# Kernel tuning notes

Measured on AMD Instinct MI355X. Metric: run time of the kernel, lower is better.

## Reference

```python
import jax, jax.numpy as jnp
import numpy as np
from jax import lax

F_DIM = 128
H_DIM = 128
K_NN = 16
S_PTS = 512
EPS = 1e-5


def _layernorm(x, g, b):
    m = jnp.mean(x, -1, keepdims=True)
    v = jnp.mean((x - m) ** 2, -1, keepdims=True)
    return (x - m) * lax.rsqrt(v + EPS) * g + b


def _batchnorm(x, g, b):
    # training-mode BN over (batch, points, neighbors) per channel; x: [B,S,K,C]
    m = jnp.mean(x, (0, 1, 2))
    v = jnp.mean((x - m) ** 2, (0, 1, 2))
    return (x - m) * lax.rsqrt(v + EPS) * g + b


def _gather(x, idx):
    # x: [B,R,C], idx: [B,...] int -> [B,...,C]
    return jax.vmap(lambda a, i: a[i])(x, idx)


def _fps(xyz, S):
    # farthest point sampling, deterministic start at index 0 (pytorch3d default)
    B, N, _ = xyz.shape
    idx0 = jnp.zeros((B,), jnp.int32)

    def step(carry, _):
        mind, last = carry
        p = jax.vmap(lambda a, i: a[i])(xyz, last)  # [B,3]
        d = jnp.sum((xyz - p[:, None]) ** 2, -1)  # [B,N]
        mind = jnp.minimum(mind, d)
        nxt = jnp.argmax(mind, -1).astype(jnp.int32)
        return (mind, nxt), nxt

    init = (jnp.full((B, N), 1e10, xyz.dtype), idx0)
    _, rest = lax.scan(step, init, None, length=S - 1)
    return jnp.concatenate([idx0[None], rest], 0).T  # [B,S]


def _knn_idx(q, ref, K):
    # squared dists [B,Q,R]; top-K nearest, sorted ascending by distance
    d2 = (jnp.sum(q * q, -1)[:, :, None] + jnp.sum(ref * ref, -1)[:, None, :]
          - 2.0 * jnp.einsum('bqd,brd->bqr', q, ref))
    _, idx = lax.top_k(-d2, K)
    return idx


def setup_inputs() -> dict:
    key = jax.random.key(0)
    ks = jax.random.split(key, 32)
    B, N, F, H = 4, 8192, F_DIM, H_DIM
    w = lambda k, shp: (jax.random.normal(k, shp, jnp.float32) * 0.02)
    return {
        'xyzp': jax.random.uniform(ks[0], (B, N, 4), jnp.float32),
        'features': jax.random.normal(ks[1], (B, N, F), jnp.float32),
        'ln_g': jnp.ones((F,), jnp.float32), 'ln_b': jnp.zeros((F,), jnp.float32),
        'td_w0': w(ks[2], (F + 3, F)), 'td_b0': jnp.zeros((F,), jnp.float32),
        'td_bn0_g': jnp.ones((F,), jnp.float32), 'td_bn0_b': jnp.zeros((F,), jnp.float32),
        'td_w1': w(ks[3], (F, F)), 'td_b1': jnp.zeros((F,), jnp.float32),
        'td_bn1_g': jnp.ones((F,), jnp.float32), 'td_bn1_b': jnp.zeros((F,), jnp.float32),
        'w_kern': w(ks[4], (F, H)), 'b_kern': jnp.zeros((H,), jnp.float32),
        'w_gkern': w(ks[5], (F, H)), 'b_gkern': jnp.zeros((H,), jnp.float32),
        'w_agg': w(ks[6], (H, F)), 'b_agg': jnp.zeros((F,), jnp.float32),
        'w_q': w(ks[7], (H, H)), 'w_k': w(ks[8], (H, H)), 'w_v': w(ks[9], (H, H)),
        'pe_w1': w(ks[10], (4, H)), 'pe_b1': jnp.zeros((H,), jnp.float32),
        'pe_w2': w(ks[11], (H, H)), 'pe_b2': jnp.zeros((H,), jnp.float32),
        'at_w1': w(ks[12], (H, H)), 'at_b1': jnp.zeros((H,), jnp.float32),
        'at_w2': w(ks[13], (H, H)), 'at_b2': jnp.zeros((H,), jnp.float32),
    }


def reference(xyzp, features, ln_g, ln_b, td_w0, td_b0, td_bn0_g, td_bn0_b,
              td_w1, td_b1, td_bn1_g, td_bn1_b, w_kern, b_kern, w_gkern, b_gkern,
              w_agg, b_agg, w_q, w_k, w_v, pe_w1, pe_b1, pe_w2, pe_b2,
              at_w1, at_b1, at_w2, at_b2):
    feats = _layernorm(features, ln_g, ln_b)
    xyz = xyzp[:, :, :3]
    # ---- TransitionDown ----
    fps_idx = _fps(xyz, S_PTS)                       # [B,S]
    new_xyz = _gather(xyz, fps_idx)                  # [B,S,3]
    idx_dn = _knn_idx(new_xyz, xyz, K_NN)            # [B,S,K]
    new_xyzp = _gather(xyzp, idx_dn)[:, :, 0]        # [B,S,4] nearest = self
    grouped_xyz = _gather(xyz, idx_dn) - new_xyz[:, :, None]   # [B,S,K,3]
    grouped_feat = _gather(feats, idx_dn)            # [B,S,K,F]
    h = jnp.concatenate([grouped_xyz, grouped_feat], -1)
    h = jax.nn.relu(_batchnorm(h @ td_w0 + td_b0, td_bn0_g, td_bn0_b))
    h = jax.nn.relu(_batchnorm(h @ td_w1 + td_b1, td_bn1_g, td_bn1_b))
    new_feats = jnp.max(h, axis=2)                   # [B,S,F]
    # ---- vector attention over K global neighbors ----
    idx_up = _knn_idx(xyz, new_xyz, K_NN)            # [B,N,K]
    pdiff = xyzp[:, :, None] - _gather(new_xyzp, idx_up)  # [B,N,K,4]
    pos_enc = jax.nn.relu(pdiff @ pe_w1 + pe_b1) @ pe_w2 + pe_b2
    x = feats @ w_kern + b_kern                      # [B,N,H]
    new_x = new_feats @ w_gkern + b_gkern            # [B,S,H]
    q = x @ w_q
    k = _gather(new_x @ w_k, idx_up)                 # [B,N,K,H]
    v = _gather(new_x @ w_v, idx_up)
    a = q[:, :, None] - k + pos_enc
    a = jax.nn.relu(a @ at_w1 + at_b1) @ at_w2 + at_b2
    a = jax.nn.softmax(a / np.float32(np.sqrt(H_DIM)), axis=2)  # softmax over neighbors
    res = jnp.sum(a * (v + pos_enc), axis=2)         # einsum bmnf,bmnf->bmf
    return res @ w_agg + b_agg + feats
```

## Files before the change

kernel.cpp:

```cpp
#include <hip/hip_runtime.h>

constexpr int B = 4, N = 8192, S = 512, K = 16, F = 128, H = 128;
constexpr float EPS = 1e-5f;

typedef short v8s __attribute__((ext_vector_type(8)));
typedef float v4f __attribute__((ext_vector_type(4)));

__device__ __forceinline__ short f2bf(float x) {
  union { float f; unsigned u; } v; v.f = x;
  unsigned r = v.u + 0x7fffu + ((v.u >> 16) & 1u);
  return (short)(r >> 16);
}
__device__ __forceinline__ float bf2f(short s) {
  union { unsigned u; float f; } v; v.u = ((unsigned)(unsigned short)s) << 16;
  return v.f;
}

template <int CTRL>
__device__ __forceinline__ float dpp_mov_f(float v) {
  return __int_as_float(__builtin_amdgcn_update_dpp(
      __float_as_int(v), __float_as_int(v), CTRL, 0xF, 0xF, false));
}
template <int CTRL>
__device__ __forceinline__ int dpp_mov_i(int v) {
  return __builtin_amdgcn_update_dpp(v, v, CTRL, 0xF, 0xF, false);
}

__global__ __launch_bounds__(256) void wconv_kernel(
    const float* __restrict__ pe_w2, const float* __restrict__ at_w1,
    const float* __restrict__ at_w2, const float* __restrict__ w_kern,
    const float* __restrict__ w_q, const float* __restrict__ td_w1,
    const float* __restrict__ td_w0, short* __restrict__ wbf) {
  int i = blockIdx.x * 256 + threadIdx.x;
  if (i < 6 * 16384) {
    int m = i >> 14, e = i & 16383;
    const float* src = m == 0 ? pe_w2 : m == 1 ? at_w1 : m == 2 ? at_w2
                     : m == 3 ? w_kern : m == 4 ? w_q : td_w1;
    int kx = e >> 7, n = e & 127;
    wbf[m * 16384 + n * 128 + kx] = f2bf(src[e]);
  } else {
    int e = i - 6 * 16384;
    int n = e / 160, kz = e % 160;
    short v = (kz < 131) ? f2bf(td_w0[kz * 128 + n]) : (short)0;
    wbf[6 * 16384 + n * 160 + kz] = v;
  }
}

__global__ __launch_bounds__(256) void ln_kernel(const float* __restrict__ features,
    const float* __restrict__ g, const float* __restrict__ bta, float* __restrict__ feats) {
  int r = blockIdx.x * 4 + (threadIdx.x >> 6);
  int lane = threadIdx.x & 63;
  const float2* fp = (const float2*)(features + (size_t)r * F);
  float2 v = fp[lane];
  float s = v.x + v.y;
  #pragma unroll
  for (int off = 32; off > 0; off >>= 1) s += __shfl_xor(s, off);
  float m = s * (1.f / F);
  float dx = v.x - m, dy = v.y - m;
  float s2 = dx * dx + dy * dy;
  #pragma unroll
  for (int off = 32; off > 0; off >>= 1) s2 += __shfl_xor(s2, off);
  float rstd = rsqrtf(s2 * (1.f / F) + EPS);
  float2 gg = ((const float2*)g)[lane];
  float2 bb = ((const float2*)bta)[lane];
  float2* op = (float2*)(feats + (size_t)r * F);
  op[lane] = make_float2(dx * rstd * gg.x + bb.x, dy * rstd * gg.y + bb.y);
}

__global__ __launch_bounds__(256, 1) void fps_kernel(const float* __restrict__ xyzp,
    float* __restrict__ new_xyz) {
  __shared__ float4 xl4[N];
  __shared__ float nx[S * 3];
  __shared__ float2 slot[2][4];
  int b = blockIdx.x, t = threadIdx.x;
  int lane = t & 63, wid = t >> 6;
  const float4* xp = (const float4*)(xyzp + (size_t)b * N * 4);
  float px[32], py[32], pz[32], mind[32];
  #pragma unroll
  for (int j = 0; j < 32; j++) {
    int idx = t + 256 * j;
    float4 p = xp[idx];
    px[j] = p.x; py[j] = p.y; pz[j] = p.z; mind[j] = 1e10f;
    xl4[idx] = p;
  }
  __syncthreads();
  float4 p0 = xl4[0];
  float cx = p0.x, cy = p0.y, cz = p0.z;
  if (t == 0) { nx[0] = cx; nx[1] = cy; nx[2] = cz; }
  for (int s = 1; s < S; ++s) {
    #pragma unroll
    for (int j = 0; j < 32; j++) {
      float dx = __fsub_rn(px[j], cx), dy = __fsub_rn(py[j], cy), dz = __fsub_rn(pz[j], cz);
      float d = __fadd_rn(__fadd_rn(__fmul_rn(dx, dx), __fmul_rn(dy, dy)), __fmul_rn(dz, dz));
      mind[j] = fminf(mind[j], d);
    }
    float a0 = fmaxf(mind[0], mind[1]),   a1 = fmaxf(mind[2], mind[3]);
    float a2 = fmaxf(mind[4], mind[5]),   a3 = fmaxf(mind[6], mind[7]);
    float a4 = fmaxf(mind[8], mind[9]),   a5 = fmaxf(mind[10], mind[11]);
    float a6 = fmaxf(mind[12], mind[13]), a7 = fmaxf(mind[14], mind[15]);
    float a8 = fmaxf(mind[16], mind[17]), a9 = fmaxf(mind[18], mind[19]);
    float aa = fmaxf(mind[20], mind[21]), ab = fmaxf(mind[22], mind[23]);
    float ac = fmaxf(mind[24], mind[25]), ad = fmaxf(mind[26], mind[27]);
    float ae = fmaxf(mind[28], mind[29]), af = fmaxf(mind[30], mind[31]);
    float b0 = fmaxf(a0, a1), b1 = fmaxf(a2, a3), b2 = fmaxf(a4, a5), b3 = fmaxf(a6, a7);
    float b4 = fmaxf(a8, a9), b5 = fmaxf(aa, ab), b6 = fmaxf(ac, ad), b7 = fmaxf(ae, af);
    float c0 = fmaxf(b0, b1), c1 = fmaxf(b2, b3), c2 = fmaxf(b4, b5), c3 = fmaxf(b6, b7);
    float e0 = fmaxf(c0, c1), e1 = fmaxf(c2, c3);
    float bv = fmaxf(e0, e1);
    unsigned msk = 0;
    #pragma unroll
    for (int j = 0; j < 32; j++) msk |= (mind[j] == bv) ? (1u << j) : 0u;
    int bj = __builtin_ctz(msk);
    int bi = t + (bj << 8);
    #define FPS_STEP(CTRL) { \
      float ov = dpp_mov_f<CTRL>(bv); int oi = dpp_mov_i<CTRL>(bi); \
      if (ov > bv || (ov == bv && oi < bi)) { bv = ov; bi = oi; } }
    FPS_STEP(0x111) FPS_STEP(0x112) FPS_STEP(0x114) FPS_STEP(0x118)
    FPS_STEP(0x142) FPS_STEP(0x143)
    #undef FPS_STEP
    int par = s & 1;
    if (lane == 63) slot[par][wid] = make_float2(bv, __int_as_float(bi));
    __syncthreads();
    float2 s0 = slot[par][0], s1 = slot[par][1], s2 = slot[par][2], s3 = slot[par][3];
    int i0 = __float_as_int(s0.y), i1 = __float_as_int(s1.y);
    int i2 = __float_as_int(s2.y), i3 = __float_as_int(s3.y);
    float4 c0v = xl4[i0], c1v = xl4[i1], c2v = xl4[i2], c3v = xl4[i3];
    float v0 = s0.x, v1 = s1.x, v2 = s2.x, v3 = s3.x;
    bool m01 = (v1 > v0) || (v1 == v0 && i1 < i0);
    float va = m01 ? v1 : v0; int ia = m01 ? i1 : i0;
    bool m23 = (v3 > v2) || (v3 == v2 && i3 < i2);
    float vb = m23 ? v3 : v2; int ib = m23 ? i3 : i2;
    bool mf = (vb > va) || (vb == va && ib < ia);
    float cax = m01 ? c1v.x : c0v.x, cay = m01 ? c1v.y : c0v.y, caz = m01 ? c1v.z : c0v.z;
    float cbx = m23 ? c3v.x : c2v.x, cby = m23 ? c3v.y : c2v.y, cbz = m23 ? c3v.z : c2v.z;
    cx = mf ? cbx : cax; cy = mf ? cby : cay; cz = mf ? cbz : caz;
    if (t == 0) { nx[s * 3 + 0] = cx; nx[s * 3 + 1] = cy; nx[s * 3 + 2] = cz; }
  }
  __syncthreads();
  for (int i = t; i < S * 3; i += 256)
    new_xyz[(size_t)b * S * 3 + i] = nx[i];
}

__global__ __launch_bounds__(256) void knn_dn_kernel(const float* __restrict__ xyzp,
    const float* __restrict__ new_xyz, int* __restrict__ idx_dn, float* __restrict__ new_xyzp) {
  int wave = threadIdx.x >> 6, lane = threadIdx.x & 63;
  int qid = blockIdx.x * 4 + wave;
  int b = qid >> 9, s = qid & (S - 1);
  const float4* xp = (const float4*)(xyzp + (size_t)b * N * 4);
  float qx = new_xyz[((size_t)b * S + s) * 3 + 0];
  float qy = new_xyz[((size_t)b * S + s) * 3 + 1];
  float qz = new_xyz[((size_t)b * S + s) * 3 + 2];
  float qq = __fadd_rn(__fadd_rn(__fmul_rn(qx, qx), __fmul_rn(qy, qy)), __fmul_rn(qz, qz));

  float lastD = -1.f; int lastI = -1;
  float curD; int curI;
  auto scan = [&]() {
    curD = 3e38f; curI = 0x7fffffff;
    for (int j = 0; j < 128; j++) {
      int i = lane + 64 * j;
      float4 p = xp[i];
      float rr  = __fadd_rn(__fadd_rn(__fmul_rn(p.x, p.x), __fmul_rn(p.y, p.y)), __fmul_rn(p.z, p.z));
      float dot = __fadd_rn(__fadd_rn(__fmul_rn(qx, p.x), __fmul_rn(qy, p.y)), __fmul_rn(qz, p.z));
      float d2 = __fsub_rn(__fadd_rn(qq, rr), __fmul_rn(2.0f, dot));
      bool gate   = (d2 > lastD) || (d2 == lastD && i > lastI);
      bool better = (d2 < curD) || (d2 == curD && i < curI);
      if (gate && better) { curD = d2; curI = i; }
    }
  };
  scan();
  int outI = 0;
  float4 nn0;
  #pragma unroll 1
  for (int r = 0; r < K; r++) {
    float mD = curD; int mI = curI; int mL = lane;
    #pragma unroll
    for (int off = 32; off > 0; off >>= 1) {
      float od = __shfl_xor(mD, off); int oi = __shfl_xor(mI, off); int ol = __shfl_xor(mL, off);
      if (od < mD || (od == mD && oi < mI)) { mD = od; mI = oi; mL = ol; }
    }
    if (lane == r) outI = mI;
    if (r == 0 && lane == 0) nn0 = xp[mI];
    if (lane == mL) { lastD = mD; lastI = mI; scan(); }
  }
  size_t base = ((size_t)b * S + s) * K;
  if (lane < K) idx_dn[base + lane] = outI;
  if (lane == 0) *(float4*)&new_xyzp[((size_t)b * S + s) * 4] = nn0;
}

__global__ __launch_bounds__(256) void knn_up_kernel(const float* __restrict__ xyzp,
    const float* __restrict__ new_xyz, int* __restrict__ idx_up) {
  int wave = threadIdx.x >> 6, lane = threadIdx.x & 63;
  int qid = blockIdx.x * 4 + wave;
  int b = qid >> 13, n = qid & (N - 1);
  const float4* xp = (const float4*)(xyzp + (size_t)b * N * 4);
  float4 qp = xp[n];
  float qx = qp.x, qy = qp.y, qz = qp.z;
  float qq = __fadd_rn(__fadd_rn(__fmul_rn(qx, qx), __fmul_rn(qy, qy)), __fmul_rn(qz, qz));
  float rx[8], ry[8], rz[8];
  #pragma unroll
  for (int j = 0; j < 8; j++) {
    int i = lane + 64 * j;
    rx[j] = new_xyz[((size_t)b * S + i) * 3 + 0];
    ry[j] = new_xyz[((size_t)b * S + i) * 3 + 1];
    rz[j] = new_xyz[((size_t)b * S + i) * 3 + 2];
  }
  float lastD = -1.f; int lastI = -1;
  float curD; int curI;
  auto scan = [&]() {
    curD = 3e38f; curI = 0x7fffffff;
    #pragma unroll
    for (int j = 0; j < 8; j++) {
      int i = lane + 64 * j;
      float rr  = __fadd_rn(__fadd_rn(__fmul_rn(rx[j], rx[j]), __fmul_rn(ry[j], ry[j])), __fmul_rn(rz[j], rz[j]));
      float dot = __fadd_rn(__fadd_rn(__fmul_rn(qx, rx[j]), __fmul_rn(qy, ry[j])), __fmul_rn(qz, rz[j]));
      float d2 = __fsub_rn(__fadd_rn(qq, rr), __fmul_rn(2.0f, dot));
      bool gate   = (d2 > lastD) || (d2 == lastD && i > lastI);
      bool better = (d2 < curD) || (d2 == curD && i < curI);
      if (gate && better) { curD = d2; curI = i; }
    }
  };
  scan();
  int outI = 0;
  #pragma unroll 1
  for (int r = 0; r < K; r++) {
    float mD = curD; int mI = curI; int mL = lane;
    #pragma unroll
    for (int off = 32; off > 0; off >>= 1) {
      float od = __shfl_xor(mD, off); int oi = __shfl_xor(mI, off); int ol = __shfl_xor(mL, off);
      if (od < mD || (od == mD && oi < mI)) { mD = od; mI = oi; mL = ol; }
    }
    if (lane == r) outI = mI;
    if (lane == mL) { lastD = mD; lastI = mI; scan(); }
  }
  size_t base = ((size_t)b * N + n) * K;
  if (lane < K) idx_up[base + lane] = outI;
}

constexpr int KS0 = 168;
__global__ __launch_bounds__(256) void td0_mfma(const float* __restrict__ xyzp,
    const float* __restrict__ new_xyz, const float* __restrict__ feats,
    const int* __restrict__ idx_dn, const short* __restrict__ w0bf, const float* __restrict__ b0,
    float* __restrict__ act0) {
  __shared__ short WT[128 * KS0];
  __shared__ short Abuf[4][16 * KS0];
  __shared__ int nbs[4][16];
  const int t = threadIdx.x, w = t >> 6, lane = t & 63;
  const int c0 = lane & 15, quad = lane >> 4;
  const int row0 = blockIdx.x * 64 + w * 16;
  const int bI = row0 >> 13;
  if (lane < 16) {
    int nb = idx_dn[row0 + lane];
    nbs[w][lane] = nb;
    int s = ((row0 + lane) >> 4) & (S - 1);
    #pragma unroll
    for (int d = 0; d < 3; d++)
      Abuf[w][lane * KS0 + d] =
          f2bf(xyzp[((size_t)bI * N + nb) * 4 + d] - new_xyz[((size_t)bI * S + s) * 3 + d]);
    for (int k2 = 131; k2 < 160; k2++) Abuf[w][lane * KS0 + k2] = 0;
  }
  #pragma unroll 4
  for (int i = 0; i < 32; i++) {
    int idx = lane + 64 * i;
    int r = idx >> 7, c = idx & 127;
    int nb = nbs[w][r];
    Abuf[w][r * KS0 + 3 + c] = f2bf(feats[((size_t)bI * N + nb) * F + c]);
  }
  #pragma unroll
  for (int i = 0; i < 10; i++) {
    int u = t + 256 * i;
    int n = u / 20, k8 = u % 20;
    *(v8s*)&WT[n * KS0 + k8 * 8] = *(const v8s*)&w0bf[n * 160 + k8 * 8];
  }
  __syncthreads();
  v4f acc[8];
  #pragma unroll
  for (int nt = 0; nt < 8; nt++) { float bvv = b0[nt * 16 + c0]; acc[nt] = (v4f){bvv, bvv, bvv, bvv}; }
  #pragma unroll
  for (int ks = 0; ks < 5; ks++) {
    v8s a = *(const v8s*)&Abuf[w][c0 * KS0 + ks * 32 + quad * 8];
    #pragma unroll
    for (int nt = 0; nt < 8; nt++) {
      v8s bf = *(const v8s*)&WT[(nt * 16 + c0) * KS0 + ks * 32 + quad * 8];
      acc[nt] = __builtin_amdgcn_mfma_f32_16x16x32_bf16(a, bf, acc[nt], 0, 0, 0);
    }
  }
  #pragma unroll
  for (int nt = 0; nt < 8; nt++)
    #pragma unroll
    for (int r = 0; r < 4; r++)
      act0[(size_t)(row0 + quad * 4 + r) * F + nt * 16 + c0] = acc[nt][r];
}

__global__ __launch_bounds__(256) void bn_reduce_kernel(const float* __restrict__ x,
                                                        float* __restrict__ sums) {
  __shared__ float ls[256], ls2[256];
  int t = threadIdx.x;
  size_t base = (size_t)blockIdx.x * 65536 + t;
  float s = 0.f, s2 = 0.f;
  for (int i = 0; i < 256; i++) {
    float v = x[base + (size_t)i * 256];
    s += v; s2 = fmaf(v, v, s2);
  }
  ls[t] = s; ls2[t] = s2; __syncthreads();
  if (t < 128) {
    s = ls[t] + ls[t + 128]; s2 = ls2[t] + ls2[t + 128];
    atomicAdd(&sums[t], s); atomicAdd(&sums[128 + t], s2);
  }
}

constexpr int KS1 = 136;
__global__ __launch_bounds__(256) void td1_mfma(const float* __restrict__ act0,
    const float* __restrict__ sums, const float* __restrict__ bn_g, const float* __restrict__ bn_b,
    const short* __restrict__ w1bf, const float* __restrict__ b1, float* __restrict__ act1) {
  __shared__ short WT[128 * KS1];
  __shared__ short Abuf[4][16 * KS1];
  __shared__ float scs[128], shs[128];
  const int t = threadIdx.x, w = t >> 6, lane = t & 63;
  const int c0 = lane & 15, quad = lane >> 4;
  const int row0 = blockIdx.x * 64 + w * 16;
  if (t < 128) {
    float m = sums[t] * (1.f / 32768.f);
    float var = sums[128 + t] * (1.f / 32768.f) - m * m;
    float rstd = rsqrtf(var + EPS);
    float sc = bn_g[t] * rstd;
    scs[t] = sc;
    shs[t] = bn_b[t] - m * sc;
  }
  #pragma unroll
  for (int i = 0; i < 8; i++) {
    int g = t + 256 * i;
    int n = g >> 4, k8 = g & 15;
    *(v8s*)&WT[n * KS1 + k8 * 8] = *(const v8s*)&w1bf[n * 128 + k8 * 8];
  }
  __syncthreads();
  #pragma unroll 4
  for (int i = 0; i < 32; i++) {
    int idx = lane + 64 * i;
    int r = idx >> 7, c = idx & 127;
    float vv = fmaxf(fmaf(act0[(size_t)(row0 + r) * F + c], scs[c], shs[c]), 0.f);
    Abuf[w][r * KS1 + c] = f2bf(vv);
  }
  v4f acc[8];
  #pragma unroll
  for (int nt = 0; nt < 8; nt++) { float bvv = b1[nt * 16 + c0]; acc[nt] = (v4f){bvv, bvv, bvv, bvv}; }
  #pragma unroll
  for (int ks = 0; ks < 4; ks++) {
    v8s a = *(const v8s*)&Abuf[w][c0 * KS1 + ks * 32 + quad * 8];
    #pragma unroll
    for (int nt = 0; nt < 8; nt++) {
      v8s bf = *(const v8s*)&WT[(nt * 16 + c0) * KS1 + ks * 32 + quad * 8];
      acc[nt] = __builtin_amdgcn_mfma_f32_16x16x32_bf16(a, bf, acc[nt], 0, 0, 0);
    }
  }
  #pragma unroll
  for (int nt = 0; nt < 8; nt++)
    #pragma unroll
    for (int r = 0; r < 4; r++)
      act1[(size_t)(row0 + quad * 4 + r) * F + nt * 16 + c0] = acc[nt][r];
}

__global__ __launch_bounds__(128) void tail_kernel(const float* __restrict__ act1,
    const float* __restrict__ sums, const float* __restrict__ bn_g, const float* __restrict__ bn_b,
    const float* __restrict__ w_gkern, const float* __restrict__ b_gkern,
    const float* __restrict__ wk, const float* __restrict__ wvp,
    float* __restrict__ kk, float* __restrict__ vv) {
  int bs = blockIdx.x, t = threadIdx.x;
  float m = sums[t] * (1.f / 32768.f);
  float var = sums[128 + t] * (1.f / 32768.f) - m * m;
  float rstd = rsqrtf(var + EPS);
  float sc = bn_g[t] * rstd;
  float sh = bn_b[t] - m * sc;
  float mx = -3e38f;
  for (int k = 0; k < K; k++) {
    float v = fmaxf(fmaf(act1[((size_t)bs * K + k) * F + t], sc, sh), 0.f);
    mx = fmaxf(mx, v);
  }
  __shared__ float row[128];
  __shared__ float row2[128];
  row[t] = mx; __syncthreads();
  float acc = b_gkern[t];
  for (int i = 0; i < F; i++) acc = fmaf(row[i], w_gkern[i * F + t], acc);
  row2[t] = acc; __syncthreads();
  float ak = 0.f, av = 0.f;
  for (int i = 0; i < F; i++) {
    float x = row2[i];
    ak = fmaf(x, wk[i * F + t], ak);
    av = fmaf(x, wvp[i * F + t], av);
  }
  kk[(size_t)bs * F + t] = ak;
  vv[(size_t)bs * F + t] = av;
}

__global__ __launch_bounds__(256) void q_mfma(const float* __restrict__ feats,
    const short* __restrict__ wkbf, const float* __restrict__ b_kern,
    const short* __restrict__ wqbf, float* __restrict__ q) {
  __shared__ short WT[128 * KS1];
  __shared__ short Abuf[4][16 * KS1];
  const int t = threadIdx.x, w = t >> 6, lane = t & 63;
  const int c0 = lane & 15, quad = lane >> 4;
  const int row0 = blockIdx.x * 64 + w * 16;
  #pragma unroll 4
  for (int i = 0; i < 32; i++) {
    int idx = lane + 64 * i;
    int r = idx >> 7, c = idx & 127;
    Abuf[w][r * KS1 + c] = f2bf(feats[(size_t)(row0 + r) * F + c]);
  }
  #pragma unroll
  for (int i = 0; i < 8; i++) {
    int g = t + 256 * i;
    int n = g >> 4, k8 = g & 15;
    *(v8s*)&WT[n * KS1 + k8 * 8] = *(const v8s*)&wkbf[n * 128 + k8 * 8];
  }
  __syncthreads();
  v4f acc[8];
  #pragma unroll
  for (int nt = 0; nt < 8; nt++) { float bvv = b_kern[nt * 16 + c0]; acc[nt] = (v4f){bvv, bvv, bvv, bvv}; }
  #pragma unroll
  for (int ks = 0; ks < 4; ks++) {
    v8s a = *(const v8s*)&Abuf[w][c0 * KS1 + ks * 32 + quad * 8];
    #pragma unroll
    for (int nt = 0; nt < 8; nt++) {
      v8s bf = *(const v8s*)&WT[(nt * 16 + c0) * KS1 + ks * 32 + quad * 8];
      acc[nt] = __builtin_amdgcn_mfma_f32_16x16x32_bf16(a, bf, acc[nt], 0, 0, 0);
    }
  }
  __syncthreads();
  #pragma unroll
  for (int i = 0; i < 8; i++) {
    int g = t + 256 * i;
    int n = g >> 4, k8 = g & 15;
    *(v8s*)&WT[n * KS1 + k8 * 8] = *(const v8s*)&wqbf[n * 128 + k8 * 8];
  }
  #pragma unroll
  for (int nt = 0; nt < 8; nt++)
    #pragma unroll
    for (int r = 0; r < 4; r++)
      Abuf[w][(quad * 4 + r) * KS1 + nt * 16 + c0] = f2bf(acc[nt][r]);
  __syncthreads();
  v4f acc2[8];
  #pragma unroll
  for (int nt = 0; nt < 8; nt++) acc2[nt] = (v4f){0.f, 0.f, 0.f, 0.f};
  #pragma unroll
  for (int ks = 0; ks < 4; ks++) {
    v8s a = *(const v8s*)&Abuf[w][c0 * KS1 + ks * 32 + quad * 8];
    #pragma unroll
    for (int nt = 0; nt < 8; nt++) {
      v8s bf = *(const v8s*)&WT[(nt * 16 + c0) * KS1 + ks * 32 + quad * 8];
      acc2[nt] = __builtin_amdgcn_mfma_f32_16x16x32_bf16(a, bf, acc2[nt], 0, 0, 0);
    }
  }
  #pragma unroll
  for (int nt = 0; nt < 8; nt++)
    #pragma unroll
    for (int r = 0; r < 4; r++)
      q[(size_t)(row0 + quad * 4 + r) * F + nt * 16 + c0] = acc2[nt][r];
}

constexpr int WS = 136;
constexpr int VS = 132;

__global__ __launch_bounds__(256) void attn_kernel(const float* __restrict__ xyzp,
    const float* __restrict__ q, const float* __restrict__ kk, const float* __restrict__ vv,
    const float* __restrict__ new_xyzp, const int* __restrict__ idx_up,
    const float* __restrict__ feats, const short* __restrict__ wbf,
    const float* __restrict__ pe_w1, const float* __restrict__ pe_b1,
    const float* __restrict__ pe_b2,
    const float* __restrict__ at_b1, const float* __restrict__ at_b2,
    const float* __restrict__ w_agg, const float* __restrict__ b_agg,
    float* __restrict__ out) {
  __shared__ short WT[128 * WS];
  __shared__ short Abuf[4][16 * WS];
  __shared__ short WVb[4][16 * VS];
  __shared__ float qsh[4][128];
  __shared__ float resh[4][128];
  __shared__ float pdsh[4][16][4];
  __shared__ int   nbsh[4][16];

  const int t = threadIdx.x, w = t >> 6, lane = t & 63;
  const int c0 = lane & 15, quad = lane >> 4;
  const int p = blockIdx.x * 4 + w;
  const int b = p >> 13;

  qsh[w][lane]      = q[(size_t)p * H + lane];
  qsh[w][lane + 64] = q[(size_t)p * H + lane + 64];
  if (lane < 16) nbsh[w][lane] = idx_up[(size_t)p * K + lane];
  {
    int k = lane >> 2, d = lane & 3;
    pdsh[w][k][d] = xyzp[(size_t)p * 4 + d] - new_xyzp[((size_t)b * S + nbsh[w][k]) * 4 + d];
  }
  #pragma unroll
  for (int cc = 0; cc < 2; cc++) {
    int c = cc * 64 + lane;
    float bb = pe_b1[c];
    float w0 = pe_w1[c], w1 = pe_w1[128 + c], w2 = pe_w1[256 + c], w3 = pe_w1[384 + c];
    #pragma unroll
    for (int k = 0; k < 16; k++) {
      float h = bb + pdsh[w][k][0] * w0 + pdsh[w][k][1] * w1 + pdsh[w][k][2] * w2 + pdsh[w][k][3] * w3;
      Abuf[w][k * WS + c] = f2bf(fmaxf(h, 0.f));
    }
  }

  auto stageW = [&](const short* __restrict__ Wt) {
    __syncthreads();
    #pragma unroll
    for (int i = 0; i < 8; i++) {
      int g = t + 256 * i;
      int n = g >> 4, k8 = g & 15;
      *(v8s*)&WT[n * WS + k8 * 8] = *(const v8s*)&Wt[n * 128 + k8 * 8];
    }
    __syncthreads();
  };
  auto gemm = [&](const float* __restrict__ bias, v4f* acc) {
    #pragma unroll
    for (int nt = 0; nt < 8; nt++) {
      float bv = bias[nt * 16 + c0];
      acc[nt] = (v4f){bv, bv, bv, bv};
    }
    #pragma unroll
    for (int ks = 0; ks < 4; ks++) {
      v8s a = *(const v8s*)&Abuf[w][c0 * WS + ks * 32 + quad * 8];
      #pragma unroll
      for (int nt = 0; nt < 8; nt++) {
        v8s bf = *(const v8s*)&WT[(nt * 16 + c0) * WS + ks * 32 + quad * 8];
        acc[nt] = __builtin_amdgcn_mfma_f32_16x16x32_bf16(a, bf, acc[nt], 0, 0, 0);
      }
    }
  };

  stageW(wbf + 0 * 16384);
  v4f pe[8];
  gemm(pe_b2, pe);

  #pragma unroll
  for (int nt = 0; nt < 8; nt++) {
    #pragma unroll
    for (int r = 0; r < 4; r++) {
      int krow = quad * 4 + r;
      int c = nt * 16 + c0;
      int nb = nbsh[w][krow];
      float pev = pe[nt][r];
      float avv = qsh[w][c] - kk[((size_t)b * S + nb) * H + c] + pev;
      float wvv = vv[((size_t)b * S + nb) * H + c] + pev;
      Abuf[w][krow * WS + c] = f2bf(avv);
      WVb[w][krow * VS + c] = f2bf(wvv);
    }
  }

  stageW(wbf + 1 * 16384);
  v4f h1[8];
  gemm(at_b1, h1);
  #pragma unroll
  for (int nt = 0; nt < 8; nt++)
    #pragma unroll
    for (int r = 0; r < 4; r++)
      Abuf[w][(quad * 4 + r) * WS + nt * 16 + c0] = f2bf(fmaxf(h1[nt][r], 0.f));

  stageW(wbf + 2 * 16384);
  v4f lg[8];
  gemm(at_b2, lg);

  const float scale = 0.08838834764831845f;
  #pragma unroll
  for (int nt = 0; nt < 8; nt++) {
    float l0 = lg[nt][0] * scale, l1 = lg[nt][1] * scale;
    float l2 = lg[nt][2] * scale, l3 = lg[nt][3] * scale;
    float m = fmaxf(fmaxf(l0, l1), fmaxf(l2, l3));
    m = fmaxf(m, __shfl_xor(m, 16));
    m = fmaxf(m, __shfl_xor(m, 32));
    float e0 = expf(l0 - m), e1 = expf(l1 - m), e2 = expf(l2 - m), e3 = expf(l3 - m);
    float ssum = e0 + e1 + e2 + e3;
    ssum += __shfl_xor(ssum, 16);
    ssum += __shfl_xor(ssum, 32);
    float inv = 1.f / ssum;
    int c = nt * 16 + c0;
    float partial =
        e0 * bf2f(WVb[w][(quad * 4 + 0) * VS + c]) + e1 * bf2f(WVb[w][(quad * 4 + 1) * VS + c]) +
        e2 * bf2f(WVb[w][(quad * 4 + 2) * VS + c]) + e3 * bf2f(WVb[w][(quad * 4 + 3) * VS + c]);
    partial += __shfl_xor(partial, 16);
    partial += __shfl_xor(partial, 32);
    if (quad == 0) resh[w][c] = partial * inv;
  }

  #pragma unroll
  for (int cc = 0; cc < 2; cc++) {
    int c = cc * 64 + lane;
    float o = b_agg[c];
    for (int i = 0; i < H; i++) o = fmaf(resh[w][i], w_agg[i * H + c], o);
    out[(size_t)p * F + c] = o + feats[(size_t)p * F + c];
  }
}

extern "C" void kernel_launch(void* const* d_in, const int* in_sizes, int n_in,
                              void* d_out, int out_size, void* d_ws, size_t ws_size,
                              hipStream_t stream) {
  (void)in_sizes; (void)n_in; (void)out_size; (void)ws_size;
  const float* xyzp    = (const float*)d_in[0];
  const float* features= (const float*)d_in[1];
  const float* ln_g    = (const float*)d_in[2];
  const float* ln_b    = (const float*)d_in[3];
  const float* td_w0   = (const float*)d_in[4];
  const float* td_b0   = (const float*)d_in[5];
  const float* bn0_g   = (const float*)d_in[6];
  const float* bn0_b   = (const float*)d_in[7];
  const float* td_w1   = (const float*)d_in[8];
  const float* td_b1   = (const float*)d_in[9];
  const float* bn1_g   = (const float*)d_in[10];
  const float* bn1_b   = (const float*)d_in[11];
  const float* w_kern  = (const float*)d_in[12];
  const float* b_kern  = (const float*)d_in[13];
  const float* w_gkern = (const float*)d_in[14];
  const float* b_gkern = (const float*)d_in[15];
  const float* w_agg   = (const float*)d_in[16];
  const float* b_agg   = (const float*)d_in[17];
  const float* w_q     = (const float*)d_in[18];
  const float* w_k     = (const float*)d_in[19];
  const float* w_v     = (const float*)d_in[20];
  const float* pe_w1   = (const float*)d_in[21];
  const float* pe_b1   = (const float*)d_in[22];
  const float* pe_w2   = (const float*)d_in[23];
  const float* pe_b2   = (const float*)d_in[24];
  const float* at_w1   = (const float*)d_in[25];
  const float* at_b1   = (const float*)d_in[26];
  const float* at_w2   = (const float*)d_in[27];
  const float* at_b2   = (const float*)d_in[28];
  float* out = (float*)d_out;

  float* wsf = (float*)d_ws;
  float* feats     = wsf + 0;
  float* q         = wsf + 4194304;
  float* act0      = wsf + 8388608;
  float* act1      = wsf + 12582912;
  short* wbf       = (short*)(wsf + 16777216);
  float* kk        = wsf + 17301504;
  float* vv        = wsf + 17563648;
  float* new_xyz   = wsf + 17825792;
  float* new_xyzp  = wsf + 17831936;
  float* sums0     = wsf + 17840128;
  float* sums1     = wsf + 17840384;
  int* idx_dn  = (int*)(wsf + 17841152);
  int* idx_up  = idx_dn + 32768;

  hipMemsetAsync(sums0, 0, 512 * sizeof(float), stream);
  wconv_kernel<<<464, 256, 0, stream>>>(pe_w2, at_w1, at_w2, w_kern, w_q, td_w1, td_w0, wbf);
  ln_kernel<<<B * N / 4, 256, 0, stream>>>(features, ln_g, ln_b, feats);
  fps_kernel<<<B, 256, 0, stream>>>(xyzp, new_xyz);
  knn_dn_kernel<<<512, 256, 0, stream>>>(xyzp, new_xyz, idx_dn, new_xyzp);
  knn_up_kernel<<<8192, 256, 0, stream>>>(xyzp, new_xyz, idx_up);
  td0_mfma<<<512, 256, 0, stream>>>(xyzp, new_xyz, feats, idx_dn, wbf + 6 * 16384, td_b0, act0);
  bn_reduce_kernel<<<64, 256, 0, stream>>>(act0, sums0);
  td1_mfma<<<512, 256, 0, stream>>>(act0, sums0, bn0_g, bn0_b, wbf + 5 * 16384, td_b1, act1);
  bn_reduce_kernel<<<64, 256, 0, stream>>>(act1, sums1);
  tail_kernel<<<B * S, 128, 0, stream>>>(act1, sums1, bn1_g, bn1_b,
      w_gkern, b_gkern, w_k, w_v, kk, vv);
  q_mfma<<<512, 256, 0, stream>>>(feats, wbf + 3 * 16384, b_kern, wbf + 4 * 16384, q);
  attn_kernel<<<8192, 256, 0, stream>>>(xyzp, q, kk, vv, new_xyzp, idx_up, feats, wbf,
      pe_w1, pe_b1, pe_b2, at_b1, at_b2, w_agg, b_agg, out);
}
```

Measured before the change: 1.779 ms.

## Track top-2 candidates in KNN scans, single-pass FPS argmax, split FMA chains

```diff
diff --git a/kernel.cpp b/kernel.cpp
--- a/kernel.cpp
+++ b/kernel.cpp
@@ -88,29 +88,14 @@
   float cx = p0.x, cy = p0.y, cz = p0.z;
   if (t == 0) { nx[0] = cx; nx[1] = cy; nx[2] = cz; }
   for (int s = 1; s < S; ++s) {
+    float bv = -1.f; int bj = 0;
     #pragma unroll
     for (int j = 0; j < 32; j++) {
       float dx = __fsub_rn(px[j], cx), dy = __fsub_rn(py[j], cy), dz = __fsub_rn(pz[j], cz);
       float d = __fadd_rn(__fadd_rn(__fmul_rn(dx, dx), __fmul_rn(dy, dy)), __fmul_rn(dz, dz));
       mind[j] = fminf(mind[j], d);
-    }
-    float a0 = fmaxf(mind[0], mind[1]),   a1 = fmaxf(mind[2], mind[3]);
-    float a2 = fmaxf(mind[4], mind[5]),   a3 = fmaxf(mind[6], mind[7]);
-    float a4 = fmaxf(mind[8], mind[9]),   a5 = fmaxf(mind[10], mind[11]);
-    float a6 = fmaxf(mind[12], mind[13]), a7 = fmaxf(mind[14], mind[15]);
-    float a8 = fmaxf(mind[16], mind[17]), a9 = fmaxf(mind[18], mind[19]);
-    float aa = fmaxf(mind[20], mind[21]), ab = fmaxf(mind[22], mind[23]);
-    float ac = fmaxf(mind[24], mind[25]), ad = fmaxf(mind[26], mind[27]);
-    float ae = fmaxf(mind[28], mind[29]), af = fmaxf(mind[30], mind[31]);
-    float b0 = fmaxf(a0, a1), b1 = fmaxf(a2, a3), b2 = fmaxf(a4, a5), b3 = fmaxf(a6, a7);
-    float b4 = fmaxf(a8, a9), b5 = fmaxf(aa, ab), b6 = fmaxf(ac, ad), b7 = fmaxf(ae, af);
-    float c0 = fmaxf(b0, b1), c1 = fmaxf(b2, b3), c2 = fmaxf(b4, b5), c3 = fmaxf(b6, b7);
-    float e0 = fmaxf(c0, c1), e1 = fmaxf(c2, c3);
-    float bv = fmaxf(e0, e1);
-    unsigned msk = 0;
-    #pragma unroll
-    for (int j = 0; j < 32; j++) msk |= (mind[j] == bv) ? (1u << j) : 0u;
-    int bj = __builtin_ctz(msk);
+      if (mind[j] > bv) { bv = mind[j]; bj = j; }
+    }
     int bi = t + (bj << 8);
     #define FPS_STEP(CTRL) { \
       float ov = dpp_mov_f<CTRL>(bv); int oi = dpp_mov_i<CTRL>(bi); \
@@ -153,26 +138,28 @@
   float qq = __fadd_rn(__fadd_rn(__fmul_rn(qx, qx), __fmul_rn(qy, qy)), __fmul_rn(qz, qz));
 
   float lastD = -1.f; int lastI = -1;
-  float curD; int curI;
-  auto scan = [&]() {
-    curD = 3e38f; curI = 0x7fffffff;
+  float D1, D2; int I1, I2;
+  auto scan2 = [&]() {
+    D1 = 3e38f; I1 = 0x7fffffff; D2 = 3e38f; I2 = 0x7fffffff;
     for (int j = 0; j < 128; j++) {
       int i = lane + 64 * j;
       float4 p = xp[i];
       float rr  = __fadd_rn(__fadd_rn(__fmul_rn(p.x, p.x), __fmul_rn(p.y, p.y)), __fmul_rn(p.z, p.z));
       float dot = __fadd_rn(__fadd_rn(__fmul_rn(qx, p.x), __fmul_rn(qy, p.y)), __fmul_rn(qz, p.z));
       float d2 = __fsub_rn(__fadd_rn(qq, rr), __fmul_rn(2.0f, dot));
-      bool gate   = (d2 > lastD) || (d2 == lastD && i > lastI);
-      bool better = (d2 < curD) || (d2 == curD && i < curI);
-      if (gate && better) { curD = d2; curI = i; }
+      bool gate = (d2 > lastD) || (d2 == lastD && i > lastI);
+      bool b1   = (d2 < D1) || (d2 == D1 && i < I1);
+      bool b2   = (d2 < D2) || (d2 == D2 && i < I2);
+      if (gate && b1)      { D2 = D1; I2 = I1; D1 = d2; I1 = i; }
+      else if (gate && b2) { D2 = d2; I2 = i; }
     }
   };
-  scan();
+  scan2();
   int outI = 0;
   float4 nn0;
   #pragma unroll 1
   for (int r = 0; r < K; r++) {
-    float mD = curD; int mI = curI; int mL = lane;
+    float mD = D1; int mI = I1; int mL = lane;
     #pragma unroll
     for (int off = 32; off > 0; off >>= 1) {
       float od = __shfl_xor(mD, off); int oi = __shfl_xor(mI, off); int ol = __shfl_xor(mL, off);
@@ -180,7 +167,11 @@
     }
     if (lane == r) outI = mI;
     if (r == 0 && lane == 0) nn0 = xp[mI];
-    if (lane == mL) { lastD = mD; lastI = mI; scan(); }
+    if (lane == mL) {
+      lastD = mD; lastI = mI;
+      if (I2 != 0x7fffffff) { D1 = D2; I1 = I2; D2 = 3e38f; I2 = 0x7fffffff; }
+      else scan2();
+    }
   }
   size_t base = ((size_t)b * S + s) * K;
   if (lane < K) idx_dn[base + lane] = outI;
@@ -205,32 +196,38 @@
     rz[j] = new_xyz[((size_t)b * S + i) * 3 + 2];
   }
   float lastD = -1.f; int lastI = -1;
-  float curD; int curI;
-  auto scan = [&]() {
-    curD = 3e38f; curI = 0x7fffffff;
+  float D1, D2; int I1, I2;
+  auto scan2 = [&]() {
+    D1 = 3e38f; I1 = 0x7fffffff; D2 = 3e38f; I2 = 0x7fffffff;
     #pragma unroll
     for (int j = 0; j < 8; j++) {
       int i = lane + 64 * j;
       float rr  = __fadd_rn(__fadd_rn(__fmul_rn(rx[j], rx[j]), __fmul_rn(ry[j], ry[j])), __fmul_rn(rz[j], rz[j]));
       float dot = __fadd_rn(__fadd_rn(__fmul_rn(qx, rx[j]), __fmul_rn(qy, ry[j])), __fmul_rn(qz, rz[j]));
       float d2 = __fsub_rn(__fadd_rn(qq, rr), __fmul_rn(2.0f, dot));
-      bool gate   = (d2 > lastD) || (d2 == lastD && i > lastI);
-      bool better = (d2 < curD) || (d2 == curD && i < curI);
-      if (gate && better) { curD = d2; curI = i; }
+      bool gate = (d2 > lastD) || (d2 == lastD && i > lastI);
+      bool b1   = (d2 < D1) || (d2 == D1 && i < I1);
+      bool b2   = (d2 < D2) || (d2 == D2 && i < I2);
+      if (gate && b1)      { D2 = D1; I2 = I1; D1 = d2; I1 = i; }
+      else if (gate && b2) { D2 = d2; I2 = i; }
     }
   };
-  scan();
+  scan2();
   int outI = 0;
   #pragma unroll 1
   for (int r = 0; r < K; r++) {
-    float mD = curD; int mI = curI; int mL = lane;
+    float mD = D1; int mI = I1; int mL = lane;
     #pragma unroll
     for (int off = 32; off > 0; off >>= 1) {
       float od = __shfl_xor(mD, off); int oi = __shfl_xor(mI, off); int ol = __shfl_xor(mL, off);
       if (od < mD || (od == mD && oi < mI)) { mD = od; mI = oi; mL = ol; }
     }
     if (lane == r) outI = mI;
-    if (lane == mL) { lastD = mD; lastI = mI; scan(); }
+    if (lane == mL) {
+      lastD = mD; lastI = mI;
+      if (I2 != 0x7fffffff) { D1 = D2; I1 = I2; D2 = 3e38f; I2 = 0x7fffffff; }
+      else scan2();
+    }
   }
   size_t base = ((size_t)b * N + n) * K;
   if (lane < K) idx_up[base + lane] = outI;
@@ -378,17 +375,39 @@
   __shared__ float row[128];
   __shared__ float row2[128];
   row[t] = mx; __syncthreads();
-  float acc = b_gkern[t];
-  for (int i = 0; i < F; i++) acc = fmaf(row[i], w_gkern[i * F + t], acc);
-  row2[t] = acc; __syncthreads();
-  float ak = 0.f, av = 0.f;
-  for (int i = 0; i < F; i++) {
-    float x = row2[i];
-    ak = fmaf(x, wk[i * F + t], ak);
-    av = fmaf(x, wvp[i * F + t], av);
-  }
-  kk[(size_t)bs * F + t] = ak;
-  vv[(size_t)bs * F + t] = av;
+  {
+    const float4* r4 = (const float4*)row;
+    float a0 = 0.f, a1 = 0.f, a2 = 0.f, a3 = 0.f;
+    #pragma unroll 8
+    for (int i = 0; i < 32; i++) {
+      float4 rv = r4[i];
+      a0 = fmaf(rv.x, w_gkern[(4 * i + 0) * F + t], a0);
+      a1 = fmaf(rv.y, w_gkern[(4 * i + 1) * F + t], a1);
+      a2 = fmaf(rv.z, w_gkern[(4 * i + 2) * F + t], a2);
+      a3 = fmaf(rv.w, w_gkern[(4 * i + 3) * F + t], a3);
+    }
+    row2[t] = b_gkern[t] + ((a0 + a1) + (a2 + a3));
+  }
+  __syncthreads();
+  {
+    const float4* r4 = (const float4*)row2;
+    float k0 = 0.f, k1 = 0.f, k2 = 0.f, k3 = 0.f;
+    float v0 = 0.f, v1 = 0.f, v2 = 0.f, v3 = 0.f;
+    #pragma unroll 4
+    for (int i = 0; i < 32; i++) {
+      float4 rv = r4[i];
+      k0 = fmaf(rv.x, wk[(4 * i + 0) * F + t], k0);
+      k1 = fmaf(rv.y, wk[(4 * i + 1) * F + t], k1);
+      k2 = fmaf(rv.z, wk[(4 * i + 2) * F + t], k2);
+      k3 = fmaf(rv.w, wk[(4 * i + 3) * F + t], k3);
+      v0 = fmaf(rv.x, wvp[(4 * i + 0) * F + t], v0);
+      v1 = fmaf(rv.y, wvp[(4 * i + 1) * F + t], v1);
+      v2 = fmaf(rv.z, wvp[(4 * i + 2) * F + t], v2);
+      v3 = fmaf(rv.w, wvp[(4 * i + 3) * F + t], v3);
+    }
+    kk[(size_t)bs * F + t] = (k0 + k1) + (k2 + k3);
+    vv[(size_t)bs * F + t] = (v0 + v1) + (v2 + v3);
+  }
 }
 
 __global__ __launch_bounds__(256) void q_mfma(const float* __restrict__ feats,
@@ -580,12 +599,22 @@
     partial += __shfl_xor(partial, 32);
     if (quad == 0) resh[w][c] = partial * inv;
   }
+  __syncthreads();
 
   #pragma unroll
   for (int cc = 0; cc < 2; cc++) {
     int c = cc * 64 + lane;
-    float o = b_agg[c];
-    for (int i = 0; i < H; i++) o = fmaf(resh[w][i], w_agg[i * H + c], o);
+    const float4* r4 = (const float4*)resh[w];
+    float o0 = 0.f, o1 = 0.f, o2 = 0.f, o3 = 0.f;
+    #pragma unroll 4
+    for (int i = 0; i < 32; i++) {
+      float4 rv = r4[i];
+      o0 = fmaf(rv.x, w_agg[(4 * i + 0) * H + c], o0);
+      o1 = fmaf(rv.y, w_agg[(4 * i + 1) * H + c], o1);
+      o2 = fmaf(rv.z, w_agg[(4 * i + 2) * H + c], o2);
+      o3 = fmaf(rv.w, w_agg[(4 * i + 3) * H + c], o3);
+    }
+    float o = b_agg[c] + ((o0 + o1) + (o2 + o3));
     out[(size_t)p * F + c] = o + feats[(size_t)p * F + c];
   }
 }
```

New measurement: 1.616 ms. -9.2%, faster.
